# Performance work log

Hardware: AMD Instinct MI355X
Metric: run time of the kernel (lower is better)

## Reference

```python
import jax, jax.numpy as jnp
import numpy as np

B = 2048    # graphs in batch
V = 15      # nodes per graph
T = 16      # window (args.n_his)
F_IN = 2    # num_features
H = 64      # nhid
LH = 40     # LSTM hidden per direction
EPER = 40   # edges per graph
N = B * V
E = B * EPER
EPS = 1e-5


def setup_inputs() -> dict:
    key = jax.random.key(0)
    ks = jax.random.split(key, 12)

    def rn(k, shape, fan_in):
        return jax.random.normal(k, shape, jnp.float32) / np.sqrt(fan_in).astype(np.float32)

    # block-diagonal batched edge_index (PyG-style batching of B graphs of V nodes)
    rng = np.random.default_rng(0)
    off = np.arange(B)[:, None] * V
    src = rng.integers(0, V, (B, EPER)) + off
    dst = rng.integers(0, V, (B, EPER)) + off
    edge_index = jnp.asarray(np.stack([src.ravel(), dst.ravel()]), dtype=jnp.int32)

    return {
        "data": jax.random.normal(ks[0], (N, F_IN, T), jnp.float32),
        "edge_attr": jax.random.uniform(ks[1], (E,), jnp.float32),
        "W1": rn(ks[2], (H, F_IN), F_IN), "b1": jnp.zeros((H,), jnp.float32),
        "Wg1": rn(ks[3], (H, H), H), "bg1": jnp.zeros((H,), jnp.float32),
        "gamma1": jnp.ones((H,), jnp.float32), "beta1": jnp.zeros((H,), jnp.float32),
        "Wg2": rn(ks[4], (H, H), H), "bg2": jnp.zeros((H,), jnp.float32),
        "gamma2": jnp.ones((H,), jnp.float32), "beta2": jnp.zeros((H,), jnp.float32),
        "Wf": rn(ks[5], (H, V * H), V * H), "bf": jnp.zeros((H,), jnp.float32),
        "Wih_f": rn(ks[6], (4 * LH, H), H), "Whh_f": rn(ks[7], (4 * LH, LH), LH),
        "bih_f": jnp.zeros((4 * LH,), jnp.float32), "bhh_f": jnp.zeros((4 * LH,), jnp.float32),
        "Wih_b": rn(ks[8], (4 * LH, H), H), "Whh_b": rn(ks[9], (4 * LH, LH), LH),
        "bih_b": jnp.zeros((4 * LH,), jnp.float32), "bhh_b": jnp.zeros((4 * LH,), jnp.float32),
        "Wc1": rn(ks[10], (16, 2 * LH), 2 * LH), "bc1": jnp.zeros((16,), jnp.float32),
        "Wc2": rn(ks[11], (1, 16), 16), "bc2": jnp.zeros((1,), jnp.float32),
        "edge_index": edge_index,
    }


def _gcn(x, W, b, edge_index, ew):
    # PyG GCNConv: linear, add self-loops (weight 1), symmetric D^-1/2 (A+I) D^-1/2.
    # x: [N, T, H] -- all T timesteps processed at once (vectorizes the source loop).
    row, col = edge_index[0], edge_index[1]
    loop = jnp.arange(N, dtype=edge_index.dtype)
    row_s = jnp.concatenate([row, loop])
    col_s = jnp.concatenate([col, loop])
    ew_s = jnp.concatenate([ew, jnp.ones((N,), ew.dtype)])
    deg = jax.ops.segment_sum(ew_s, col_s, num_segments=N)
    dinv = jnp.where(deg > 0, jax.lax.rsqrt(deg), 0.0)
    norm = dinv[row_s] * ew_s * dinv[col_s]                      # [E+N]
    xw = jnp.einsum('nth,hk->ntk', x, W)                          # [N, T, H]
    agg = jax.ops.segment_sum(norm[:, None, None] * xw[row_s], col_s, num_segments=N)
    return agg + b


def _bn(x, gamma, beta):
    # BatchNorm1d training-mode stats, per timestep (axis 0 = nodes), biased var.
    m = x.mean(axis=0)
    v = x.var(axis=0)
    return gamma * (x - m) * jax.lax.rsqrt(v + EPS) + beta


def _lstm(X, Wih, Whh, bih, bhh):
    # X: [T, B, H]; PyTorch gate order i, f, g, o.
    def step(carry, xt):
        h, c = carry
        g = xt @ Wih.T + h @ Whh.T + (bih + bhh)
        i, f, gg, o = jnp.split(g, 4, axis=-1)
        c = jax.nn.sigmoid(f) * c + jax.nn.sigmoid(i) * jnp.tanh(gg)
        h = jax.nn.sigmoid(o) * jnp.tanh(c)
        return (h, c), h
    h0 = jnp.zeros((X.shape[1], LH), X.dtype)
    _, hs = jax.lax.scan(step, (h0, h0), X)
    return hs


def _forward(data, edge_attr, W1, b1, Wg1, bg1, gamma1, beta1, Wg2, bg2, gamma2, beta2,
             Wf, bf, Wih_f, Whh_f, bih_f, bhh_f, Wih_b, Whh_b, bih_b, bhh_b,
             Wc1, bc1, Wc2, bc2, edge_index):
    # conv_1 (1x1 Conv2d) == per-node linear over features, kept per timestep
    x = jnp.einsum('nft,hf->nth', data, W1) + b1                 # [N, T, H]
    # Hierarchical GCN with residuals (ReLU then BN, per the source)
    x1 = _bn(jax.nn.relu(_gcn(x, Wg1, bg1, edge_index, edge_attr)), gamma1, beta1) + x
    x2 = _bn(jax.nn.relu(_gcn(x1, Wg2, bg2, edge_index, edge_attr)), gamma2, beta2) + x1
    # stack over timesteps -> [T, B, V*H]
    Xs = x2.transpose(1, 0, 2).reshape(T, B, V * H)
    Xs = jax.nn.relu(Xs @ Wf.T + bf)                             # fc1 -> [T, B, H]
    hs_f = _lstm(Xs, Wih_f, Whh_f, bih_f, bhh_f)
    hs_b = _lstm(Xs[::-1], Wih_b, Whh_b, bih_b, bhh_b)
    # r_out[-1] = [fwd h at t=T-1, bwd h at t=T-1 (first step of reversed scan)]
    last = jnp.concatenate([hs_f[-1], hs_b[0]], axis=-1)          # [B, 80]
    hcls = jax.nn.relu(last @ Wc1.T + bc1)                        # dropout inactive (eval)
    return hcls @ Wc2.T + bc2                                     # [B, 1]


def reference(data, edge_attr, W1, b1, Wg1, bg1, gamma1, beta1, Wg2, bg2, gamma2, beta2,
              Wf, bf, Wih_f, Whh_f, bih_f, bhh_f, Wih_b, Whh_b, bih_b, bhh_b,
              Wc1, bc1, Wc2, bc2, edge_index):
    return _forward(data, edge_attr, W1, b1, Wg1, bg1, gamma1, beta1, Wg2, bg2,
                    gamma2, beta2, Wf, bf, Wih_f, Whh_f, bih_f, bhh_f,
                    Wih_b, Whh_b, bih_b, bhh_b, Wc1, bc1, Wc2, bc2, edge_index)
```

## Files before the change

### kernel.cpp

```cpp
#include <hip/hip_runtime.h>

typedef unsigned int u32;
typedef unsigned short u16;
typedef __attribute__((ext_vector_type(8))) short bf16x8;
typedef __attribute__((ext_vector_type(4))) float f32x4;

#define NB   2048
#define NV   15
#define NT   16
#define NH   64
#define NLH  40
#define EPER 40
#define NN   (NB*NV)
#define NE   (NB*EPER)

#define F_DATA 0
#define F_EA   983040
#define P_W1   1064960
#define P_B1   1065088
#define P_WG1  1065152
#define P_BG1  1069248
#define P_G1   1069312
#define P_BE1  1069376
#define P_WG2  1069440
#define P_BG2  1073536
#define P_G2   1073600
#define P_BE2  1073664
#define P_WF   1073728
#define P_BF   1135168
#define P_WIHF 1135232
#define P_WHHF 1145472
#define P_BIHF 1151872
#define P_BHHF 1152032
#define P_WIHB 1152192
#define P_WHHB 1162432
#define P_BIHB 1168832
#define P_BHHB 1168992
#define P_WC1  1169152
#define P_BC1  1170432
#define P_WC2  1170448
#define P_BC2  1170464
#define CVT_TOTAL 1170465
#define WFB_OFF   1170496
#define WIHT_OFF  1205504
#define STATS_OFF 1231936
#define XS_OFF    1240128
#define FLAG_OFF  3337280
#define BUFX_BYTE 13349376
#define BUFY_BYTE 76263936

__device__ const int d_cum[27] = {
  0, 983040, 1064960, 1065088, 1065152, 1069248, 1069312, 1069376,
  1069440, 1073536, 1073600, 1073664, 1073728, 1135168, 1135232, 1145472,
  1151872, 1152032, 1152192, 1162432, 1168832, 1168992, 1169152, 1170432,
  1170448, 1170464, 1170465};

struct Ptrs { const void* p[26]; };

__device__ inline float b2f(u16 u) { return __uint_as_float(((u32)u) << 16); }
__device__ inline u16 f2b(float f) {
  u32 u = __float_as_uint(f);
  u32 r = (u + 0x7FFFu + ((u >> 16) & 1u)) >> 16;
  return (u16)r;
}
__device__ inline float sigf(float x) { return 1.0f / (1.0f + __expf(-x)); }

__global__ void k_detect(const u16* __restrict__ raw, int* __restrict__ flag) {
  __shared__ int bad;
  if (threadIdx.x == 0) bad = 0;
  __syncthreads();
  for (int i = threadIdx.x; i < 4096; i += 256) {
    float f = b2f(raw[i]);
    if (!(fabsf(f) < 1000.0f)) atomicOr(&bad, 1);
  }
  __syncthreads();
  if (threadIdx.x == 0) *flag = bad ? 0 : 1;
}

__global__ void k_convert(Ptrs ptrs, float* __restrict__ W) {
  int gid = blockIdx.x * 256 + threadIdx.x;
  if (gid >= CVT_TOTAL) return;
  int flag = *(const int*)(W + FLAG_OFF);
  int ti = 0;
  #pragma unroll
  for (int i = 1; i < 26; ++i) ti += (gid >= d_cum[i]);
  int j = gid - d_cum[ti];
  const void* src = ptrs.p[ti];
  W[gid] = flag ? b2f(((const u16*)src)[j]) : ((const float*)src)[j];
}

__global__ void k_preswz(float* __restrict__ W, u16* __restrict__ WfB) {
  int i = blockIdx.x * 256 + threadIdx.x;
  if (i < 61440) {
    int j = i & 7, lane = (i >> 3) & 63, kt = (i >> 9) & 3, ks = i >> 11;
    int kout = kt * 16 + (lane & 15);
    int m = ks * 32 + ((lane >> 4) << 3) + j;
    WfB[i] = f2b(W[P_WF + kout * 960 + m]);
  } else if (i < 69632) {
    int ii = i - 61440;
    int L = ii >> 12, r = ii & 4095;
    int j = r & 7, lane = (r >> 3) & 63, nt = (r >> 9) & 3, ks = (r >> 11) & 1;
    int h = ks * 32 + ((lane >> 4) << 3) + j;
    int k = nt * 16 + (lane & 15);
    WfB[i] = f2b(W[(L ? P_WG2 : P_WG1) + h * 64 + k]);
  } else if (i < 90112) {
    int e = i - 69632;
    int which = e / 10240, rem = e % 10240;
    int kk = rem / 160, jj = rem % 160;
    W[WIHT_OFF + e] = W[(which ? P_WIHB : P_WIHF) + jj * 64 + kk];
  }
}

template<int LAYER>
__global__ __launch_bounds__(256, 4)
void k_gcn(const float* __restrict__ W, const int* __restrict__ ei,
           const u16* __restrict__ bufIn, u16* __restrict__ bufOut,
           const u16* __restrict__ WgB,
           float* __restrict__ S1, float* __restrict__ S2,
           int bgoff, int scoff, int shoff) {
  __shared__ u16 s_x[15360];
  __shared__ float s_m[240];
  __shared__ float s_deg[16];
  __shared__ float s_d[480];
  __shared__ float s_w1[192];

  int g = blockIdx.x, tid = threadIdx.x;

  uint4 ld[8];
  if (LAYER == 2) {
    const uint4* py = (const uint4*)(bufIn + g * 15360);
    #pragma unroll
    for (int c = 0; c < 7; ++c) ld[c] = py[tid + c * 256];
    if (tid < 128) ld[7] = py[tid + 1792];
  }

  float ew = 0.f; int er = 0, ec = 0;
  if (tid < 40) {
    er = ei[g * 40 + tid] - g * 15;
    ec = ei[NE + g * 40 + tid] - g * 15;
    ew = W[F_EA + g * 40 + tid];
  }
  if (tid >= 40 && tid < 56) s_deg[tid - 40] = 1.0f;
  for (int i = tid; i < 240; i += 256) s_m[i] = 0.f;
  if (tid >= 64 && tid < 184) ((float4*)s_d)[tid - 64] = ((const float4*)(W + F_DATA + g * 480))[tid - 64];
  if (tid >= 192 && tid < 240) ((float4*)s_w1)[tid - 192] = ((const float4*)(W + P_W1))[tid - 192];
  __syncthreads();

  if (tid < 40) atomicAdd(&s_deg[ec], ew);
  #pragma unroll
  for (int c = 0; c < 8; ++c) {
    if (c < 7 || tid < 128) {
      int i = tid + c * 256;
      int v = i >> 7, rem = i & 127, t = rem >> 3, q = rem & 7;
      int h0 = q * 8;
      float d0 = s_d[v * 32 + t], d1 = s_d[v * 32 + 16 + t];
      u32 pk[4];
      if (LAYER == 1) {
        #pragma unroll
        for (int jp = 0; jp < 4; ++jp) {
          int h = h0 + jp * 2;
          float xa = fmaf(d0, s_w1[2 * h],     fmaf(d1, s_w1[2 * h + 1], s_w1[128 + h]));
          float xb = fmaf(d0, s_w1[2 * h + 2], fmaf(d1, s_w1[2 * h + 3], s_w1[129 + h]));
          pk[jp] = (u32)f2b(xa) | ((u32)f2b(xb) << 16);
        }
      } else {
        u32 uys[4] = {ld[c].x, ld[c].y, ld[c].z, ld[c].w};
        int th0 = t * 64 + h0;
        float4 A0 = *(const float4*)(W + scoff + th0), A1 = *(const float4*)(W + scoff + th0 + 4);
        float4 B0 = *(const float4*)(W + shoff + th0), B1 = *(const float4*)(W + shoff + th0 + 4);
        float scs[8] = {A0.x, A0.y, A0.z, A0.w, A1.x, A1.y, A1.z, A1.w};
        float shs[8] = {B0.x, B0.y, B0.z, B0.w, B1.x, B1.y, B1.z, B1.w};
        #pragma unroll
        for (int jp = 0; jp < 4; ++jp) {
          int j0 = jp * 2, h = h0 + j0;
          float xa = fmaf(d0, s_w1[2 * h],     fmaf(d1, s_w1[2 * h + 1], s_w1[128 + h]));
          float xb = fmaf(d0, s_w1[2 * h + 2], fmaf(d1, s_w1[2 * h + 3], s_w1[129 + h]));
          float a = fmaf(b2f((u16)(uys[jp] & 0xffff)), scs[j0],     shs[j0])     + xa;
          float b = fmaf(b2f((u16)(uys[jp] >> 16)),    scs[j0 + 1], shs[j0 + 1]) + xb;
          pk[jp] = (u32)f2b(a) | ((u32)f2b(b) << 16);
        }
      }
      u32 byte = ((u32)(i * 16)) ^ (((u32)(t & 7)) << 4);
      *(uint4*)((char*)s_x + byte) = make_uint4(pk[0], pk[1], pk[2], pk[3]);
    }
  }
  __syncthreads();
  if (tid < 15) s_deg[tid] = rsqrtf(s_deg[tid]);
  __syncthreads();
  if (tid < 40) atomicAdd(&s_m[ec * 16 + er], s_deg[er] * ew * s_deg[ec]);
  if (tid >= 64 && tid < 80) {
    float dv = s_deg[tid - 64];
    atomicAdd(&s_m[(tid - 64) * 17], dv * dv);
  }
  __syncthreads();

  u32* sx32 = (u32*)s_x;
  {
    float x0[15], x1[15], x2[15], x3[15];
    int p0 = tid, p1 = tid + 256;
    int t0 = p0 >> 5, h0 = (2 * p0) & 63;
    int t1 = p1 >> 5, h1 = (2 * p1) & 63;
    u32 ba0 = ((u32)(t0 * 128 + h0 * 2)) ^ (((u32)(t0 & 7)) << 4);
    u32 ba1 = ((u32)(t1 * 128 + h1 * 2)) ^ (((u32)(t1 & 7)) << 4);
    #pragma unroll
    for (int v = 0; v < 15; ++v) {
      u32 ua = sx32[(ba0 + v * 2048) >> 2];
      u32 ub = sx32[(ba1 + v * 2048) >> 2];
      x0[v] = b2f((u16)(ua & 0xffff)); x1[v] = b2f((u16)(ua >> 16));
      x2[v] = b2f((u16)(ub & 0xffff)); x3[v] = b2f((u16)(ub >> 16));
    }
    #pragma unroll
    for (int vc = 0; vc < 15; ++vc) {
      float a0 = 0.f, a1 = 0.f, a2 = 0.f, a3 = 0.f;
      #pragma unroll
      for (int vr = 0; vr < 15; ++vr) {
        float m = s_m[vc * 16 + vr];
        a0 = fmaf(m, x0[vr], a0); a1 = fmaf(m, x1[vr], a1);
        a2 = fmaf(m, x2[vr], a2); a3 = fmaf(m, x3[vr], a3);
      }
      sx32[(ba0 + vc * 2048) >> 2] = (u32)f2b(a0) | ((u32)f2b(a1) << 16);
      sx32[(ba1 + vc * 2048) >> 2] = (u32)f2b(a2) | ((u32)f2b(a3) << 16);
    }
  }
  __syncthreads();

  int wid = tid >> 6, lane = tid & 63;
  int tA = lane & 15, kg = lane >> 4;
  const bf16x8* wb = (const bf16x8*)WgB;
  bf16x8 bf0 = wb[(0 * 4 + wid) * 64 + lane];
  bf16x8 bf1 = wb[(1 * 4 + wid) * 64 + lane];
  int kout = wid * 16 + tA;
  float bias = W[bgoff + kout];
  f32x4 acc[15];
  #pragma unroll
  for (int v = 0; v < 15; ++v) acc[v] = (f32x4){0.f, 0.f, 0.f, 0.f};
  u32 sw = ((u32)(tA & 7)) << 4;
  #pragma unroll
  for (int v = 0; v < 15; ++v) {
    u32 bb = (u32)(v * 2048 + tA * 128 + kg * 16);
    bf16x8 a0 = *(const bf16x8*)(s_x + ((bb ^ sw) >> 1));
    bf16x8 a1 = *(const bf16x8*)(s_x + (((bb + 64) ^ sw) >> 1));
    acc[v] = __builtin_amdgcn_mfma_f32_16x16x32_bf16(a0, bf0, acc[v], 0, 0, 0);
    acc[v] = __builtin_amdgcn_mfma_f32_16x16x32_bf16(a1, bf1, acc[v], 0, 0, 0);
  }

  float s1r[4] = {0.f, 0.f, 0.f, 0.f}, s2r[4] = {0.f, 0.f, 0.f, 0.f};
  __syncthreads();
  #pragma unroll
  for (int v = 0; v < 15; ++v) {
    #pragma unroll
    for (int r = 0; r < 4; ++r) {
      float y = fmaxf(acc[v][r] + bias, 0.f);
      int t = kg * 4 + r;
      u32 byte = ((u32)(v * 2048 + t * 128 + kout * 2)) ^ (((u32)kg) << 5);
      *(u16*)((char*)s_x + byte) = f2b(y);
      s1r[r] += y; s2r[r] += y * y;
    }
  }
  __syncthreads();
  uint4* dst = (uint4*)(bufOut + g * 15360);
  const uint4* src = (const uint4*)s_x;
  #pragma unroll
  for (int c = 0; c < 8; ++c) {
    if (c < 7 || tid < 128) {
      int i = tid + c * 256;
      dst[i] = src[i ^ (((i >> 5) & 3) << 1)];
    }
  }
  #pragma unroll
  for (int r = 0; r < 4; ++r) {
    int idx = (kg * 4 + r) * 64 + kout;
    atomicAdd(&S1[idx], s1r[r]);
    atomicAdd(&S2[idx], s2r[r]);
  }
}

__global__ void k_finalize(float* __restrict__ W, int layer) {
  int i = blockIdx.x * 256 + threadIdx.x;
  if (i >= 1024) return;
  int base = STATS_OFF + (layer == 1 ? 0 : 2048);
  int scb  = STATS_OFF + (layer == 1 ? 4096 : 6144);
  float m   = W[base + i] * (1.0f / 30720.0f);
  float var = W[base + 1024 + i] * (1.0f / 30720.0f) - m * m;
  float istd = rsqrtf(var + 1e-5f);
  int h = i & 63;
  float gm = W[(layer == 1 ? P_G1 : P_G2) + h];
  float bt = W[(layer == 1 ? P_BE1 : P_BE2) + h];
  float sc = gm * istd;
  W[scb + i] = sc;
  W[scb + 1024 + i] = bt - m * sc;
}

__global__ __launch_bounds__(256, 4)
void k_fc1(const float* __restrict__ W, const u16* __restrict__ bufY2,
           const u16* __restrict__ bufY1, const u16* __restrict__ WfB,
           float* __restrict__ Xs) {
  __shared__ u16 s_x[15360];
  __shared__ float s_d[480];
  __shared__ float s_w1[192];
  int g = blockIdx.x, tid = threadIdx.x;
  if (tid < 120) ((float4*)s_d)[tid] = ((const float4*)(W + F_DATA + g * 480))[tid];
  if (tid >= 128 && tid < 176) ((float4*)s_w1)[tid - 128] = ((const float4*)(W + P_W1))[tid - 128];
  __syncthreads();
  const uint4* py2 = (const uint4*)(bufY2 + g * 15360);
  const uint4* py1 = (const uint4*)(bufY1 + g * 15360);
  #pragma unroll
  for (int c = 0; c < 8; ++c) {
    if (c < 7 || tid < 128) {
      int i = tid + c * 256;
      int v = i >> 7, rem = i & 127, t = rem >> 3, q = rem & 7;
      int h0 = q * 8, th0 = t * 64 + h0;
      uint4 u2 = py2[i], u1 = py1[i];
      u32 u2s[4] = {u2.x, u2.y, u2.z, u2.w}, u1s[4] = {u1.x, u1.y, u1.z, u1.w};
      float d0 = s_d[v * 32 + t], d1 = s_d[v * 32 + 16 + t];
      float4 A0 = *(const float4*)(W + STATS_OFF + 6144 + th0), A1 = *(const float4*)(W + STATS_OFF + 6148 + th0);
      float4 B0 = *(const float4*)(W + STATS_OFF + 7168 + th0), B1 = *(const float4*)(W + STATS_OFF + 7172 + th0);
      float4 C0 = *(const float4*)(W + STATS_OFF + 4096 + th0), C1 = *(const float4*)(W + STATS_OFF + 4100 + th0);
      float4 D0 = *(const float4*)(W + STATS_OFF + 5120 + th0), D1 = *(const float4*)(W + STATS_OFF + 5124 + th0);
      float sc2[8] = {A0.x, A0.y, A0.z, A0.w, A1.x, A1.y, A1.z, A1.w};
      float sh2[8] = {B0.x, B0.y, B0.z, B0.w, B1.x, B1.y, B1.z, B1.w};
      float sc1[8] = {C0.x, C0.y, C0.z, C0.w, C1.x, C1.y, C1.z, C1.w};
      float sh1[8] = {D0.x, D0.y, D0.z, D0.w, D1.x, D1.y, D1.z, D1.w};
      u32 pk[4];
      #pragma unroll
      for (int jp = 0; jp < 4; ++jp) {
        int j0 = jp * 2, h = h0 + j0;
        float xa = fmaf(d0, s_w1[2 * h],     fmaf(d1, s_w1[2 * h + 1], s_w1[128 + h]));
        float xb = fmaf(d0, s_w1[2 * h + 2], fmaf(d1, s_w1[2 * h + 3], s_w1[129 + h]));
        float x1a = fmaf(b2f((u16)(u1s[jp] & 0xffff)), sc1[j0],     sh1[j0])     + xa;
        float x1b = fmaf(b2f((u16)(u1s[jp] >> 16)),    sc1[j0 + 1], sh1[j0 + 1]) + xb;
        float a = fmaf(b2f((u16)(u2s[jp] & 0xffff)), sc2[j0],     sh2[j0])     + x1a;
        float b = fmaf(b2f((u16)(u2s[jp] >> 16)),    sc2[j0 + 1], sh2[j0 + 1]) + x1b;
        pk[jp] = (u32)f2b(a) | ((u32)f2b(b) << 16);
      }
      u32 byte = ((u32)(i * 16)) ^ (((u32)(t & 7)) << 4);
      *(uint4*)((char*)s_x + byte) = make_uint4(pk[0], pk[1], pk[2], pk[3]);
    }
  }
  __syncthreads();

  int wid = tid >> 6, lane = tid & 63;
  int tA = lane & 15, kg = lane >> 4;
  f32x4 acc = {0.f, 0.f, 0.f, 0.f};
  const bf16x8* wf = (const bf16x8*)WfB;
  #pragma unroll 2
  for (int ks = 0; ks < 30; ++ks) {
    int v = ks >> 1, half = ks & 1;
    u32 byte = (u32)(v * 2048 + tA * 128 + (half * 32 + kg * 8) * 2) ^ (((u32)(tA & 7)) << 4);
    bf16x8 afrag = *(const bf16x8*)(s_x + (byte >> 1));
    bf16x8 bfrag = wf[(ks * 4 + wid) * 64 + lane];
    acc = __builtin_amdgcn_mfma_f32_16x16x32_bf16(afrag, bfrag, acc, 0, 0, 0);
  }
  int kout = wid * 16 + (lane & 15);
  float bias = W[P_BF + kout];
  #pragma unroll
  for (int r = 0; r < 4; ++r) {
    int t = (lane >> 4) * 4 + r;
    Xs[t * 131072 + g * 64 + kout] = fmaxf(acc[r] + bias, 0.0f);
  }
}

__global__ __launch_bounds__(512)
void k_lstm2(const float* __restrict__ W, const float* __restrict__ Xs,
             void* __restrict__ dout, const int* __restrict__ flagp) {
  extern __shared__ float smem[];
  float* s_whh = smem;
  float* s_xs  = smem + 6480;
  float* s_h   = smem + 14672;
  float* s_c   = smem + 14992;
  float* s_hb  = smem + 15312;
  float* s_g   = smem + 15632;
  float* s_cls = smem + 16912;
  int tid = threadIdx.x, r0 = blockIdx.x * 8;

  for (int i = tid; i < 6400; i += 512) {
    int jj = i / 40, kk = i % 40;
    s_whh[kk * 162 + jj] = W[P_WHHF + i];
  }
  #pragma unroll
  for (int c = 0; c < 4; ++c) {
    int i4 = tid + c * 512;
    int i = i4 * 4;
    int t = i >> 9, b = (i >> 6) & 7, k = i & 63;
    ((float4*)s_xs)[i4] = *(const float4*)(Xs + t * 131072 + (r0 + b) * 64 + k);
  }
  if (tid < 320) { s_h[tid] = 0.f; s_c[tid] = 0.f; }
  __syncthreads();

  int r = tid >> 6, l = tid & 63;
  int l2 = (l < 32) ? l + 128 : l;
  float G0[16], G1[16], G2[16];
  {
    float b0 = W[P_BIHF + l]      + W[P_BHHF + l];
    float b1 = W[P_BIHF + l + 64] + W[P_BHHF + l + 64];
    float b2 = W[P_BIHF + l2]     + W[P_BHHF + l2];
    #pragma unroll
    for (int t = 0; t < 16; ++t) { G0[t] = b0; G1[t] = b1; G2[t] = b2; }
    const float* wih = W + WIHT_OFF;
    const float* xr = s_xs + r * 64;
    for (int kk = 0; kk < 64; ++kk) {
      float w0 = wih[kk * 160 + l];
      float w1 = wih[kk * 160 + l + 64];
      float w2 = wih[kk * 160 + l2];
      #pragma unroll
      for (int t = 0; t < 16; ++t) {
        float xv = xr[t * 512 + kk];
        G0[t] = fmaf(xv, w0, G0[t]);
        G1[t] = fmaf(xv, w1, G1[t]);
        G2[t] = fmaf(xv, w2, G2[t]);
      }
    }
  }

  #pragma unroll
  for (int t = 0; t < 16; ++t) {
    float acc0 = G0[t], acc1 = G1[t], acc2 = G2[t];
    const float* hr = s_h + r * 40;
    #pragma unroll 8
    for (int kk = 0; kk < 40; ++kk) {
      float hv = hr[kk];
      acc0 = fmaf(hv, s_whh[kk * 162 + l], acc0);
      acc1 = fmaf(hv, s_whh[kk * 162 + l + 64], acc1);
      acc2 = fmaf(hv, s_whh[kk * 162 + l2], acc2);
    }
    s_g[r * 160 + l] = acc0;
    s_g[r * 160 + l + 64] = acc1;
    if (l < 32) s_g[r * 160 + l2] = acc2;
    __syncthreads();
    if (tid < 320) {
      int row = tid / 40, jj = tid % 40;
      const float* gr = s_g + row * 160;
      float ig = gr[jj], fg = gr[jj + 40], gg = gr[jj + 80], og = gr[jj + 120];
      float c = sigf(fg) * s_c[tid] + sigf(ig) * tanhf(gg);
      s_c[tid] = c;
      s_h[tid] = sigf(og) * tanhf(c);
    }
    __syncthreads();
  }

  if (tid < 320) {
    int row = tid / 40, jj = tid % 40;
    const float* wb = W + WIHT_OFF + 10240;
    float ai = W[P_BIHB + jj]       + W[P_BHHB + jj];
    float ag = W[P_BIHB + jj + 80]  + W[P_BHHB + jj + 80];
    float ao = W[P_BIHB + jj + 120] + W[P_BHHB + jj + 120];
    const float* xr = s_xs + 15 * 512 + row * 64;
    for (int kk = 0; kk < 64; ++kk) {
      float xv = xr[kk];
      ai = fmaf(xv, wb[kk * 160 + jj], ai);
      ag = fmaf(xv, wb[kk * 160 + jj + 80], ag);
      ao = fmaf(xv, wb[kk * 160 + jj + 120], ao);
    }
    float c = sigf(ai) * tanhf(ag);
    s_hb[tid] = sigf(ao) * tanhf(c);
  }
  __syncthreads();

  if (tid < 128) {
    int rr = tid >> 4, jj = tid & 15;
    float a = W[P_BC1 + jj];
    for (int p = 0; p < 40; ++p) a = fmaf(W[P_WC1 + jj * 80 + p],      s_h[rr * 40 + p],  a);
    for (int p = 0; p < 40; ++p) a = fmaf(W[P_WC1 + jj * 80 + 40 + p], s_hb[rr * 40 + p], a);
    s_cls[rr * 16 + jj] = fmaxf(a, 0.0f);
  }
  __syncthreads();
  if (tid < 8) {
    float o = W[P_BC2];
    #pragma unroll
    for (int jj = 0; jj < 16; ++jj) o = fmaf(W[P_WC2 + jj], s_cls[tid * 16 + jj], o);
    if (*flagp) ((u16*)dout)[r0 + tid] = f2b(o);
    else        ((float*)dout)[r0 + tid] = o;
  }
}

extern "C" void kernel_launch(void* const* d_in, const int* in_sizes, int n_in,
                              void* d_out, int out_size, void* d_ws, size_t ws_size,
                              hipStream_t stream) {
  float* W = (float*)d_ws;
  u16* bufX = (u16*)((char*)d_ws + BUFX_BYTE);
  u16* bufY = (u16*)((char*)d_ws + BUFY_BYTE);
  u16* WfB  = (u16*)(W + WFB_OFF);
  const int* ei = (const int*)d_in[26];

  (void)hipFuncSetAttribute(reinterpret_cast<const void*>(&k_lstm2),
                            hipFuncAttributeMaxDynamicSharedMemorySize, 68160);

  hipMemsetAsync(W + STATS_OFF, 0, 4096 * sizeof(float), stream);
  k_detect<<<1, 256, 0, stream>>>((const u16*)d_in[0], (int*)(W + FLAG_OFF));
  Ptrs ptrs;
  for (int i = 0; i < 26; ++i) ptrs.p[i] = d_in[i];
  k_convert<<<(CVT_TOTAL + 255) / 256, 256, 0, stream>>>(ptrs, W);
  k_preswz<<<352, 256, 0, stream>>>(W, WfB);
  k_gcn<1><<<NB, 256, 0, stream>>>(W, ei, nullptr, bufY, WfB + 61440,
      W + STATS_OFF, W + STATS_OFF + 1024, P_BG1, 0, 0);
  k_finalize<<<4, 256, 0, stream>>>(W, 1);
  k_gcn<2><<<NB, 256, 0, stream>>>(W, ei, bufY, bufX, WfB + 65536,
      W + STATS_OFF + 2048, W + STATS_OFF + 3072, P_BG2,
      STATS_OFF + 4096, STATS_OFF + 5120);
  k_finalize<<<4, 256, 0, stream>>>(W, 2);
  k_fc1<<<NB, 256, 0, stream>>>(W, bufX, bufY, WfB, W + XS_OFF);
  k_lstm2<<<256, 512, 68160, stream>>>(W, W + XS_OFF, d_out, (const int*)(W + FLAG_OFF));
}
```

Measured before the change: 337.0 us.

## Use 512-thread blocks, reorder GCN to transform-then-aggregate, split fc1 K across waves

The GCN kernels now run with 512 threads. They apply the weight MFMA first and do the adjacency aggregation afterward. The aggregation step fuses bias, ReLU, the global store and the BN statistics, so the separate write-back pass through shared memory is gone. fc1 splits its 30 K-steps across two wave groups and reduces the partial sums through shared memory. The aim is more parallelism per graph and fewer serialized LDS passes. In exchange it adds an extra barrier and possible occupancy limits from the larger blocks, and the aggregation now runs on bf16-rounded transformed features.

```diff
diff --git a/kernel.cpp b/kernel.cpp
--- a/kernel.cpp
+++ b/kernel.cpp
@@ -112,7 +112,7 @@
 }
 
 template<int LAYER>
-__global__ __launch_bounds__(256, 4)
+__global__ __launch_bounds__(512)
 void k_gcn(const float* __restrict__ W, const int* __restrict__ ei,
            const u16* __restrict__ bufIn, u16* __restrict__ bufOut,
            const u16* __restrict__ WgB,
@@ -126,12 +126,12 @@
 
   int g = blockIdx.x, tid = threadIdx.x;
 
-  uint4 ld[8];
+  uint4 ld[4];
   if (LAYER == 2) {
     const uint4* py = (const uint4*)(bufIn + g * 15360);
     #pragma unroll
-    for (int c = 0; c < 7; ++c) ld[c] = py[tid + c * 256];
-    if (tid < 128) ld[7] = py[tid + 1792];
+    for (int c = 0; c < 3; ++c) ld[c] = py[tid + c * 512];
+    if (tid < 384) ld[3] = py[tid + 1536];
   }
 
   float ew = 0.f; int er = 0, ec = 0;
@@ -141,16 +141,16 @@
     ew = W[F_EA + g * 40 + tid];
   }
   if (tid >= 40 && tid < 56) s_deg[tid - 40] = 1.0f;
-  for (int i = tid; i < 240; i += 256) s_m[i] = 0.f;
+  for (int i = tid; i < 240; i += 512) s_m[i] = 0.f;
   if (tid >= 64 && tid < 184) ((float4*)s_d)[tid - 64] = ((const float4*)(W + F_DATA + g * 480))[tid - 64];
   if (tid >= 192 && tid < 240) ((float4*)s_w1)[tid - 192] = ((const float4*)(W + P_W1))[tid - 192];
   __syncthreads();
 
   if (tid < 40) atomicAdd(&s_deg[ec], ew);
   #pragma unroll
-  for (int c = 0; c < 8; ++c) {
-    if (c < 7 || tid < 128) {
-      int i = tid + c * 256;
+  for (int c = 0; c < 4; ++c) {
+    if (c < 3 || tid < 384) {
+      int i = tid + c * 512;
       int v = i >> 7, rem = i & 127, t = rem >> 3, q = rem & 7;
       int h0 = q * 8;
       float d0 = s_d[v * 32 + t], d1 = s_d[v * 32 + 16 + t];
@@ -194,84 +194,78 @@
   }
   __syncthreads();
 
-  u32* sx32 = (u32*)s_x;
+  int wid8 = tid >> 6, lane = tid & 63;
+  int wid4 = wid8 & 3, vh = wid8 >> 2;
+  int tA = lane & 15, kg = lane >> 4;
+  const bf16x8* wb = (const bf16x8*)WgB;
+  bf16x8 bf0 = wb[(0 * 4 + wid4) * 64 + lane];
+  bf16x8 bf1 = wb[(1 * 4 + wid4) * 64 + lane];
+  int v0 = vh * 8, nv = vh ? 7 : 8;
+  f32x4 acc[8];
+  #pragma unroll
+  for (int vv = 0; vv < 8; ++vv) acc[vv] = (f32x4){0.f, 0.f, 0.f, 0.f};
+  u32 sw = ((u32)(tA & 7)) << 4;
+  #pragma unroll
+  for (int vv = 0; vv < 8; ++vv) {
+    if (vv < nv) {
+      int v = v0 + vv;
+      u32 bb = (u32)(v * 2048 + tA * 128 + kg * 16);
+      bf16x8 a0 = *(const bf16x8*)(s_x + ((bb ^ sw) >> 1));
+      bf16x8 a1 = *(const bf16x8*)(s_x + (((bb + 64) ^ sw) >> 1));
+      acc[vv] = __builtin_amdgcn_mfma_f32_16x16x32_bf16(a0, bf0, acc[vv], 0, 0, 0);
+      acc[vv] = __builtin_amdgcn_mfma_f32_16x16x32_bf16(a1, bf1, acc[vv], 0, 0, 0);
+    }
+  }
+  __syncthreads();
+
   {
-    float x0[15], x1[15], x2[15], x3[15];
-    int p0 = tid, p1 = tid + 256;
-    int t0 = p0 >> 5, h0 = (2 * p0) & 63;
-    int t1 = p1 >> 5, h1 = (2 * p1) & 63;
-    u32 ba0 = ((u32)(t0 * 128 + h0 * 2)) ^ (((u32)(t0 & 7)) << 4);
-    u32 ba1 = ((u32)(t1 * 128 + h1 * 2)) ^ (((u32)(t1 & 7)) << 4);
+    int kout = wid4 * 16 + tA;
+    #pragma unroll
+    for (int vv = 0; vv < 8; ++vv) {
+      if (vv < nv) {
+        int v = v0 + vv;
+        #pragma unroll
+        for (int r = 0; r < 4; ++r) {
+          int t = kg * 4 + r;
+          u32 byte = ((u32)(v * 2048 + t * 128 + kout * 2)) ^ (((u32)kg) << 5);
+          *(u16*)((char*)s_x + byte) = f2b(acc[vv][r]);
+        }
+      }
+    }
+  }
+  __syncthreads();
+
+  {
+    int t = tid >> 5, c32 = tid & 31;
+    int k = c32 * 2;
+    u32 swz = ((u32)(t >> 2)) << 5;
+    float z0[15], z1[15];
     #pragma unroll
     for (int v = 0; v < 15; ++v) {
-      u32 ua = sx32[(ba0 + v * 2048) >> 2];
-      u32 ub = sx32[(ba1 + v * 2048) >> 2];
-      x0[v] = b2f((u16)(ua & 0xffff)); x1[v] = b2f((u16)(ua >> 16));
-      x2[v] = b2f((u16)(ub & 0xffff)); x3[v] = b2f((u16)(ub >> 16));
-    }
+      u32 u = *(const u32*)((const char*)s_x + (((u32)(v * 2048 + t * 128 + c32 * 4)) ^ swz));
+      z0[v] = b2f((u16)(u & 0xffff));
+      z1[v] = b2f((u16)(u >> 16));
+    }
+    float bg0 = W[bgoff + k], bg1 = W[bgoff + k + 1];
+    float s1a = 0.f, s1b = 0.f, s2a = 0.f, s2b = 0.f;
+    u32* gout = (u32*)(bufOut + g * 15360);
     #pragma unroll
     for (int vc = 0; vc < 15; ++vc) {
-      float a0 = 0.f, a1 = 0.f, a2 = 0.f, a3 = 0.f;
+      float a0 = 0.f, a1 = 0.f;
+      const float* mr = s_m + vc * 16;
       #pragma unroll
       for (int vr = 0; vr < 15; ++vr) {
-        float m = s_m[vc * 16 + vr];
-        a0 = fmaf(m, x0[vr], a0); a1 = fmaf(m, x1[vr], a1);
-        a2 = fmaf(m, x2[vr], a2); a3 = fmaf(m, x3[vr], a3);
+        float m = mr[vr];
+        a0 = fmaf(m, z0[vr], a0);
+        a1 = fmaf(m, z1[vr], a1);
       }
-      sx32[(ba0 + vc * 2048) >> 2] = (u32)f2b(a0) | ((u32)f2b(a1) << 16);
-      sx32[(ba1 + vc * 2048) >> 2] = (u32)f2b(a2) | ((u32)f2b(a3) << 16);
-    }
-  }
-  __syncthreads();
-
-  int wid = tid >> 6, lane = tid & 63;
-  int tA = lane & 15, kg = lane >> 4;
-  const bf16x8* wb = (const bf16x8*)WgB;
-  bf16x8 bf0 = wb[(0 * 4 + wid) * 64 + lane];
-  bf16x8 bf1 = wb[(1 * 4 + wid) * 64 + lane];
-  int kout = wid * 16 + tA;
-  float bias = W[bgoff + kout];
-  f32x4 acc[15];
-  #pragma unroll
-  for (int v = 0; v < 15; ++v) acc[v] = (f32x4){0.f, 0.f, 0.f, 0.f};
-  u32 sw = ((u32)(tA & 7)) << 4;
-  #pragma unroll
-  for (int v = 0; v < 15; ++v) {
-    u32 bb = (u32)(v * 2048 + tA * 128 + kg * 16);
-    bf16x8 a0 = *(const bf16x8*)(s_x + ((bb ^ sw) >> 1));
-    bf16x8 a1 = *(const bf16x8*)(s_x + (((bb + 64) ^ sw) >> 1));
-    acc[v] = __builtin_amdgcn_mfma_f32_16x16x32_bf16(a0, bf0, acc[v], 0, 0, 0);
-    acc[v] = __builtin_amdgcn_mfma_f32_16x16x32_bf16(a1, bf1, acc[v], 0, 0, 0);
-  }
-
-  float s1r[4] = {0.f, 0.f, 0.f, 0.f}, s2r[4] = {0.f, 0.f, 0.f, 0.f};
-  __syncthreads();
-  #pragma unroll
-  for (int v = 0; v < 15; ++v) {
-    #pragma unroll
-    for (int r = 0; r < 4; ++r) {
-      float y = fmaxf(acc[v][r] + bias, 0.f);
-      int t = kg * 4 + r;
-      u32 byte = ((u32)(v * 2048 + t * 128 + kout * 2)) ^ (((u32)kg) << 5);
-      *(u16*)((char*)s_x + byte) = f2b(y);
-      s1r[r] += y; s2r[r] += y * y;
-    }
-  }
-  __syncthreads();
-  uint4* dst = (uint4*)(bufOut + g * 15360);
-  const uint4* src = (const uint4*)s_x;
-  #pragma unroll
-  for (int c = 0; c < 8; ++c) {
-    if (c < 7 || tid < 128) {
-      int i = tid + c * 256;
-      dst[i] = src[i ^ (((i >> 5) & 3) << 1)];
-    }
-  }
-  #pragma unroll
-  for (int r = 0; r < 4; ++r) {
-    int idx = (kg * 4 + r) * 64 + kout;
-    atomicAdd(&S1[idx], s1r[r]);
-    atomicAdd(&S2[idx], s2r[r]);
+      float y0 = fmaxf(a0 + bg0, 0.f), y1 = fmaxf(a1 + bg1, 0.f);
+      gout[vc * 512 + t * 32 + c32] = (u32)f2b(y0) | ((u32)f2b(y1) << 16);
+      s1a += y0; s1b += y1; s2a += y0 * y0; s2b += y1 * y1;
+    }
+    int idx = t * 64 + k;
+    atomicAdd(&S1[idx], s1a);     atomicAdd(&S1[idx + 1], s1b);
+    atomicAdd(&S2[idx], s2a);     atomicAdd(&S2[idx + 1], s2b);
   }
 }
 
@@ -291,7 +285,7 @@
   W[scb + 1024 + i] = bt - m * sc;
 }
 
-__global__ __launch_bounds__(256, 4)
+__global__ __launch_bounds__(512)
 void k_fc1(const float* __restrict__ W, const u16* __restrict__ bufY2,
            const u16* __restrict__ bufY1, const u16* __restrict__ WfB,
            float* __restrict__ Xs) {
@@ -305,9 +299,9 @@
   const uint4* py2 = (const uint4*)(bufY2 + g * 15360);
   const uint4* py1 = (const uint4*)(bufY1 + g * 15360);
   #pragma unroll
-  for (int c = 0; c < 8; ++c) {
-    if (c < 7 || tid < 128) {
-      int i = tid + c * 256;
+  for (int c = 0; c < 4; ++c) {
+    if (c < 3 || tid < 384) {
+      int i = tid + c * 512;
       int v = i >> 7, rem = i & 127, t = rem >> 3, q = rem & 7;
       int h0 = q * 8, th0 = t * 64 + h0;
       uint4 u2 = py2[i], u1 = py1[i];
@@ -339,24 +333,33 @@
   }
   __syncthreads();
 
-  int wid = tid >> 6, lane = tid & 63;
+  int wid8 = tid >> 6, lane = tid & 63;
+  int wid4 = wid8 & 3, kh = wid8 >> 2;
   int tA = lane & 15, kg = lane >> 4;
   f32x4 acc = {0.f, 0.f, 0.f, 0.f};
   const bf16x8* wf = (const bf16x8*)WfB;
-  #pragma unroll 2
-  for (int ks = 0; ks < 30; ++ks) {
+  #pragma unroll 3
+  for (int s = 0; s < 15; ++s) {
+    int ks = kh * 15 + s;
     int v = ks >> 1, half = ks & 1;
     u32 byte = (u32)(v * 2048 + tA * 128 + (half * 32 + kg * 8) * 2) ^ (((u32)(tA & 7)) << 4);
     bf16x8 afrag = *(const bf16x8*)(s_x + (byte >> 1));
-    bf16x8 bfrag = wf[(ks * 4 + wid) * 64 + lane];
+    bf16x8 bfrag = wf[(ks * 4 + wid4) * 64 + lane];
     acc = __builtin_amdgcn_mfma_f32_16x16x32_bf16(afrag, bfrag, acc, 0, 0, 0);
   }
-  int kout = wid * 16 + (lane & 15);
-  float bias = W[P_BF + kout];
-  #pragma unroll
-  for (int r = 0; r < 4; ++r) {
-    int t = (lane >> 4) * 4 + r;
-    Xs[t * 131072 + g * 64 + kout] = fmaxf(acc[r] + bias, 0.0f);
+  __syncthreads();
+  float* s_xf = (float*)s_x;
+  if (kh == 1) *(f32x4*)(s_xf + (wid4 * 64 + lane) * 4) = acc;
+  __syncthreads();
+  if (kh == 0) {
+    f32x4 other = *(const f32x4*)(s_xf + (wid4 * 64 + lane) * 4);
+    int kout = wid4 * 16 + tA;
+    float bias = W[P_BF + kout];
+    #pragma unroll
+    for (int r = 0; r < 4; ++r) {
+      int t = kg * 4 + r;
+      Xs[t * 131072 + g * 64 + kout] = fmaxf(acc[r] + other[r] + bias, 0.0f);
+    }
   }
 }
 
@@ -491,13 +494,13 @@
   for (int i = 0; i < 26; ++i) ptrs.p[i] = d_in[i];
   k_convert<<<(CVT_TOTAL + 255) / 256, 256, 0, stream>>>(ptrs, W);
   k_preswz<<<352, 256, 0, stream>>>(W, WfB);
-  k_gcn<1><<<NB, 256, 0, stream>>>(W, ei, nullptr, bufY, WfB + 61440,
+  k_gcn<1><<<NB, 512, 0, stream>>>(W, ei, nullptr, bufY, WfB + 61440,
       W + STATS_OFF, W + STATS_OFF + 1024, P_BG1, 0, 0);
   k_finalize<<<4, 256, 0, stream>>>(W, 1);
-  k_gcn<2><<<NB, 256, 0, stream>>>(W, ei, bufY, bufX, WfB + 65536,
+  k_gcn<2><<<NB, 512, 0, stream>>>(W, ei, bufY, bufX, WfB + 65536,
       W + STATS_OFF + 2048, W + STATS_OFF + 3072, P_BG2,
       STATS_OFF + 4096, STATS_OFF + 5120);
   k_finalize<<<4, 256, 0, stream>>>(W, 2);
-  k_fc1<<<NB, 256, 0, stream>>>(W, bufX, bufY, WfB, W + XS_OFF);
+  k_fc1<<<NB, 512, 0, stream>>>(W, bufX, bufY, WfB, W + XS_OFF);
   k_lstm2<<<256, 512, 68160, stream>>>(W, W + XS_OFF, d_out, (const int*)(W + FLAG_OFF));
 }
```

Result: slower. 440.8 us (+30.8%).
